# Optimization experiments

Hardware: AMD Instinct MI355X
Metric: run time of the kernel (lower is better)

The kernel has to match this reference:

```python
import jax, jax.numpy as jnp
import numpy as np

N = 30000   # nodes
E = 480000  # directed edges (avg degree 16)
CIN = 64    # c_in
CH = 64     # c_hidden

_PARAM_NAMES = ["Wl1","bl1","Wr1","br1","We1","att1","bo1",
                "Wlm","blm","Wrm","brm","Wem","attm","bom",
                "Wl8","bl8","Wr8","br8","We8","att8","bo8"]
_PARAM_SHAPES = [(CIN,CH),(CH,),(CIN,CH),(CH,),(1,CH),(CH,),(CH,),
                 (6,CH,CH),(6,CH),(6,CH,CH),(6,CH),(6,1,CH),(6,CH),(6,CH),
                 (CH,1),(1,),(CH,1),(1,),(1,1),(1,),(1,)]

def setup_inputs() -> dict:
    key = jax.random.key(0)
    ks = jax.random.split(key, 4 + len(_PARAM_NAMES))
    inp = {
        "features": jax.random.normal(ks[0], (N, CIN), dtype=jnp.float32),
        "edge_src": jax.random.randint(ks[1], (E,), 0, N),
        "edge_dst": jax.random.randint(ks[2], (E,), 0, N),
        "edge_weight": jax.random.uniform(ks[3], (E,), dtype=jnp.float32),
    }
    for i, (name, shape) in enumerate(zip(_PARAM_NAMES, _PARAM_SHAPES)):
        inp[name] = jax.random.normal(ks[4 + i], shape, dtype=jnp.float32) * 0.05
    return inp

def _gatv2_layer(x, src, dst, attr, Wl, bl, Wr, br, We, att, bo):
    # PyG GATv2Conv, heads=1, negative_slope=0.2; (src,dst,attr) already include self-loops.
    n = x.shape[0]
    xl = x @ Wl + bl                                  # [N, C] source-side transform (lin_l)
    xr = x @ Wr + br                                  # [N, C] target-side transform (lin_r)
    e = xl[src] + xr[dst] + attr[:, None] * We[0]     # [Ea, C] per-edge pre-activation
    logit = jax.nn.leaky_relu(e, 0.2) @ att           # [Ea]
    m = jax.ops.segment_max(logit, dst, num_segments=n)
    z = jnp.exp(logit - m[dst])                       # stable softmax over each node's in-edges
    s = jax.ops.segment_sum(z, dst, num_segments=n)
    alpha = z / s[dst]                                # [Ea]
    return jax.ops.segment_sum(alpha[:, None] * xl[src], dst, num_segments=n) + bo

def reference(features, edge_src, edge_dst, edge_weight,
              Wl1, bl1, Wr1, br1, We1, att1, bo1,
              Wlm, blm, Wrm, brm, Wem, attm, bom,
              Wl8, bl8, Wr8, br8, We8, att8, bo8):
    n = features.shape[0]
    # add_self_loops=True with fill_value='mean': self-loop attr = mean of incoming edge attrs
    cnt = jax.ops.segment_sum(jnp.ones_like(edge_weight), edge_dst, num_segments=n)
    loop_attr = jax.ops.segment_sum(edge_weight, edge_dst, num_segments=n) / jnp.maximum(cnt, 1.0)
    loops = jnp.arange(n)
    src = jnp.concatenate([edge_src, loops])
    dst = jnp.concatenate([edge_dst, loops])
    attr = jnp.concatenate([edge_weight, loop_attr])
    x = _gatv2_layer(features, src, dst, attr, Wl1, bl1, Wr1, br1, We1, att1, bo1)
    for i in range(6):  # conv2..conv7, structurally identical hidden layers
        x = _gatv2_layer(x, src, dst, attr, Wlm[i], blm[i], Wrm[i], brm[i], Wem[i], attm[i], bom[i])
    x = _gatv2_layer(x, src, dst, attr, Wl8, bl8, Wr8, br8, We8, att8, bo8)  # [N, 1]
    return jnp.mean(x, axis=-2)  # mean pool over nodes -> [1]
```

## Files before the change

kernel.cpp:

```cpp
#include <hip/hip_runtime.h>
#include <hip/hip_fp16.h>
#include <math.h>

#define CH 64

__device__ __forceinline__ void multi_reduce8(const float lv[8], float L[8], int lane) {
  bool b5 = (lane & 32) != 0;
  float r1[4];
#pragma unroll
  for (int j = 0; j < 4; ++j) {
    float keep = b5 ? lv[j + 4] : lv[j];
    float send = b5 ? lv[j] : lv[j + 4];
    r1[j] = keep + __shfl_xor(send, 32, 64);
  }
  bool b4 = (lane & 16) != 0;
  float r2[2];
#pragma unroll
  for (int j = 0; j < 2; ++j) {
    float keep = b4 ? r1[j + 2] : r1[j];
    float send = b4 ? r1[j] : r1[j + 2];
    r2[j] = keep + __shfl_xor(send, 16, 64);
  }
  bool b3 = (lane & 8) != 0;
  float keep = b3 ? r2[1] : r2[0];
  float send = b3 ? r2[0] : r2[1];
  float v = keep + __shfl_xor(send, 8, 64);
  v += __shfl_xor(v, 4, 64);
  v += __shfl_xor(v, 2, 64);
  v += __shfl_xor(v, 1, 64);
#pragma unroll
  for (int j = 0; j < 8; ++j) L[j] = __shfl(v, j * 8, 64);
}

struct AggState {
  float m, s, acc;
};

__device__ __forceinline__ void agg_batch8(const float xv[8], const int2& ed, int e, int nc,
                                           float Wec, float attc, float xrc, int lane,
                                           AggState& st) {
  float lv[8], L[8];
#pragma unroll
  for (int j = 0; j < 8; ++j) {
    float aj = __int_as_float(__shfl(ed.y, e + j, 64));
    float ee = fmaf(aj, Wec, xv[j] + xrc);
    lv[j] = (ee > 0.f ? ee : 0.2f * ee) * attc;
  }
  multi_reduce8(lv, L, lane);
#pragma unroll
  for (int j = 0; j < 8; ++j)
    if (e + j >= nc) L[j] = -INFINITY;
  float bm = fmaxf(fmaxf(fmaxf(L[0], L[1]), fmaxf(L[2], L[3])),
                   fmaxf(fmaxf(L[4], L[5]), fmaxf(L[6], L[7])));
  float mn = fmaxf(st.m, bm);
  float sc = __expf(st.m - mn);
  float psum = 0.f, pdot = 0.f;
#pragma unroll
  for (int j = 0; j < 8; ++j) {
    float p = __expf(L[j] - mn);
    psum += p;
    pdot = fmaf(p, xv[j], pdot);
  }
  st.s = fmaf(st.s, sc, psum);
  st.acc = fmaf(st.acc, sc, pdot);
  st.m = mn;
}

#define LOAD8(dst, ebase)                                          \
  {                                                                \
    _Pragma("unroll") for (int j = 0; j < 8; ++j) {                \
      int sj = __shfl(ed.x, (ebase) + j, 64);                      \
      dst[j] = __half2float(xlh[(size_t)sj * CH + lane]);          \
    }                                                              \
  }

__device__ __forceinline__ AggState agg_node(const __half* __restrict__ xlh,
                                             const int2* __restrict__ csr, int beg, int dv,
                                             float Wec, float attc, float xrc, int lane) {
  AggState st;
  st.m = -INFINITY;
  st.s = 0.f;
  st.acc = 0.f;
  for (int chunk = 0; chunk < dv; chunk += 64) {
    int nc = min(64, dv - chunk);
    int2 ed = (lane < nc) ? csr[beg + chunk + lane] : make_int2(0, 0);
    float xva[8], xvb[8];
    LOAD8(xva, 0);
    int e = 0;
    for (;;) {
      if (e + 8 < nc) LOAD8(xvb, e + 8);
      agg_batch8(xva, ed, e, nc, Wec, attc, xrc, lane, st);
      e += 8;
      if (e >= nc) break;
      if (e + 8 < nc) LOAD8(xva, e + 8);
      agg_batch8(xvb, ed, e, nc, Wec, attc, xrc, lane, st);
      e += 8;
      if (e >= nc) break;
    }
  }
  return st;
}


#define WSUM_SCALE 33554432.0f
#define WSUM_MASK 0xFFFFFFFFFFULL

__global__ void k_count(const int* __restrict__ dst, const float* __restrict__ w, int E,
                        unsigned long long* __restrict__ agg, int* __restrict__ rank) {
  int i = blockIdx.x * blockDim.x + threadIdx.x;
  if (i < E) {
    int d = dst[i];
    unsigned long long pk = (1ULL << 40) | (unsigned long long)(w[i] * WSUM_SCALE);
    unsigned long long old = atomicAdd(&agg[d], pk);
    rank[i] = (int)(old >> 40);
  }
}

__global__ void k_alloc(const unsigned long long* __restrict__ agg,
                        float* __restrict__ loop_attr, int* __restrict__ deg,
                        int* __restrict__ row_beg, int* __restrict__ total, int n) {
  int i = blockIdx.x * blockDim.x + threadIdx.x;
  int lane = threadIdx.x & 63;
  int d = 0;
  if (i < n) {
    unsigned long long v = agg[i];
    int c = (int)(v >> 40);
    float ws = (float)(v & WSUM_MASK) * (1.0f / WSUM_SCALE);
    loop_attr[i] = ws / fmaxf((float)c, 1.0f);
    d = c + 1;
    deg[i] = d;
  }
  int x = d;
#pragma unroll
  for (int off = 1; off < 64; off <<= 1) {
    int t = __shfl_up(x, off, 64);
    if (lane >= off) x += t;
  }
  int base = 0;
  if (lane == 63) base = atomicAdd(total, x);
  base = __shfl(base, 63, 64);
  if (i < n) row_beg[i] = base + x - d;
}

__global__ void k_scatter(const int* __restrict__ src, const int* __restrict__ dst,
                          const float* __restrict__ w, const int* __restrict__ rank, int E,
                          const int* __restrict__ row_beg, int2* __restrict__ csr) {
  int i = blockIdx.x * blockDim.x + threadIdx.x;
  if (i < E) {
    int d = dst[i];
    csr[row_beg[d] + rank[i]] = make_int2(src[i], __float_as_int(w[i]));
  }
}

__global__ void k_selfloop(int n, const int* __restrict__ row_beg, const int* __restrict__ deg,
                           int2* __restrict__ csr, const float* __restrict__ loop_attr) {
  int v = blockIdx.x * blockDim.x + threadIdx.x;
  if (v < n) {
    csr[row_beg[v] + deg[v] - 1] = make_int2(v, __float_as_int(loop_attr[v]));
  }
}


__global__ void __launch_bounds__(256) k_transform(
    const float* __restrict__ x, const float* __restrict__ Wl, const float* __restrict__ bl,
    const float* __restrict__ Wr, const float* __restrict__ br,
    __half* __restrict__ xlh, float* __restrict__ xr, int n) {
  __shared__ float sW[2][CH * CH];
  for (int i = threadIdx.x; i < (CH * CH) / 4; i += blockDim.x) {
    ((float4*)sW[0])[i] = ((const float4*)Wl)[i];
    ((float4*)sW[1])[i] = ((const float4*)Wr)[i];
  }
  __syncthreads();
  int lane = threadIdx.x & 63;
  int wid = threadIdx.x >> 6;
  float blc = bl[lane], brc = br[lane];
  int wavesPerGrid = (gridDim.x * blockDim.x) >> 6;
  for (int row = blockIdx.x * (blockDim.x >> 6) + wid; row < n; row += wavesPerGrid) {
    float xv = x[(size_t)row * CH + lane];
    float accl = blc, accr = brc;
#pragma unroll
    for (int k = 0; k < CH; ++k) {
      float xk = __shfl(xv, k, 64);
      accl = fmaf(xk, sW[0][k * CH + lane], accl);
      accr = fmaf(xk, sW[1][k * CH + lane], accr);
    }
    xlh[(size_t)row * CH + lane] = __float2half(accl);
    xr[(size_t)row * CH + lane] = accr;
  }
}


__global__ void __launch_bounds__(256) k_aggregate(
    const __half* __restrict__ xlh, const float* __restrict__ xr,
    const int* __restrict__ row_beg, const int* __restrict__ deg,
    const int2* __restrict__ csr,
    const float* __restrict__ We, const float* __restrict__ att, const float* __restrict__ bo,
    float* __restrict__ out, int n) {
  int lane = threadIdx.x & 63;
  int v = (blockIdx.x * blockDim.x + threadIdx.x) >> 6;
  if (v >= n) return;
  float Wec = We[lane], attc = att[lane], boc = bo[lane];
  float xrc = xr[(size_t)v * CH + lane];
  AggState st = agg_node(xlh, csr, row_beg[v], deg[v], Wec, attc, xrc, lane);
  out[(size_t)v * CH + lane] = st.acc / st.s + boc;
}

__global__ void __launch_bounds__(256) k_aggregate_t8(
    const __half* __restrict__ xlh, const float* __restrict__ xr,
    const int* __restrict__ row_beg, const int* __restrict__ deg,
    const int2* __restrict__ csr,
    const float* __restrict__ We, const float* __restrict__ att, const float* __restrict__ bo,
    const float* __restrict__ Wl8, const float* __restrict__ bl8,
    const float* __restrict__ Wr8, const float* __restrict__ br8,
    float* __restrict__ xl8, float* __restrict__ xr8, int n) {
  int lane = threadIdx.x & 63;
  int v = (blockIdx.x * blockDim.x + threadIdx.x) >> 6;
  if (v >= n) return;
  float Wec = We[lane], attc = att[lane], boc = bo[lane];
  float xrc = xr[(size_t)v * CH + lane];
  AggState st = agg_node(xlh, csr, row_beg[v], deg[v], Wec, attc, xrc, lane);
  float orow = st.acc / st.s + boc;
  float a = orow * Wl8[lane];
  float b = orow * Wr8[lane];
#pragma unroll
  for (int off = 32; off > 0; off >>= 1) {
    a += __shfl_xor(a, off, 64);
    b += __shfl_xor(b, off, 64);
  }
  if (lane == 0) {
    xl8[v] = a + bl8[0];
    xr8[v] = b + br8[0];
  }
}

__global__ void __launch_bounds__(256) k_agg8_mean(
    const float* __restrict__ xl8, const float* __restrict__ xr8,
    const int* __restrict__ row_beg, const int* __restrict__ deg,
    const int2* __restrict__ csr,
    const float* __restrict__ We, const float* __restrict__ att, const float* __restrict__ bo,
    float* __restrict__ out, int n) {
  int lane = threadIdx.x & 63;
  int wid = threadIdx.x >> 6;
  float We0 = We[0], att0 = att[0], bo0 = bo[0];
  float inv_n = 1.0f / (float)n;
  float local = 0.f;
  int nwaves = gridDim.x * 4;
  for (int v = blockIdx.x * 4 + wid; v < n; v += nwaves) {
    float xrc = xr8[v];
    int beg = row_beg[v], dv = deg[v];
    float m = -INFINITY, s = 0.f, acc = 0.f;
    for (int chunk = 0; chunk < dv; chunk += 64) {
      int idx = chunk + lane;
      bool valid = idx < dv;
      int2 ed = valid ? csr[beg + idx] : make_int2(0, 0);
      float xlc = valid ? xl8[ed.x] : 0.f;
      float ee = fmaf(__int_as_float(ed.y), We0, xlc + xrc);
      float logit = valid ? (ee > 0.f ? ee : 0.2f * ee) * att0 : -INFINITY;
      float bm = logit;
#pragma unroll
      for (int off = 32; off > 0; off >>= 1) bm = fmaxf(bm, __shfl_xor(bm, off, 64));
      float mn = fmaxf(m, bm);
      float p = __expf(logit - mn);
      float pd = p * xlc;
#pragma unroll
      for (int off = 32; off > 0; off >>= 1) {
        p += __shfl_xor(p, off, 64);
        pd += __shfl_xor(pd, off, 64);
      }
      float sc = __expf(m - mn);
      s = fmaf(s, sc, p);
      acc = fmaf(acc, sc, pd);
      m = mn;
    }
    local += (acc / s + bo0) * inv_n;
  }
  __shared__ float sw[4];
  if (lane == 0) sw[wid] = local;
  __syncthreads();
  if (threadIdx.x == 0) atomicAdd(out, sw[0] + sw[1] + sw[2] + sw[3]);
}


extern "C" void kernel_launch(void* const* d_in, const int* in_sizes, int n_in,
                              void* d_out, int out_size, void* d_ws, size_t ws_size,
                              hipStream_t stream) {
  const float* features = (const float*)d_in[0];
  const int* edge_src = (const int*)d_in[1];
  const int* edge_dst = (const int*)d_in[2];
  const float* edge_w = (const float*)d_in[3];
  const int N = in_sizes[0] / CH;
  const int E = in_sizes[1];

  char* p = (char*)d_ws;
  auto take = [&](size_t bytes) {
    char* r = p;
    p += (bytes + 255) & ~(size_t)255;
    return r;
  };
  float* xA = (float*)take((size_t)N * CH * 4);
  float* xB = (float*)take((size_t)N * CH * 4);
  __half* xlh = (__half*)take((size_t)N * CH * 2);
  float* xr = (float*)take((size_t)N * CH * 4);
  int2* csr = (int2*)take((size_t)(E + N) * 8);
  char* zero_region = take((size_t)N * 8 + 256);
  unsigned long long* agg = (unsigned long long*)zero_region;
  int* total = (int*)(zero_region + (size_t)N * 8);
  int* rank = (int*)take((size_t)E * 4);
  float* loop_attr = (float*)take((size_t)N * 4);
  int* deg = (int*)take((size_t)N * 4);
  int* row_beg = (int*)take((size_t)N * 4);
  float* xl8 = (float*)take((size_t)N * 4);
  float* xr8 = (float*)take((size_t)N * 4);

  hipMemsetAsync(zero_region, 0, (size_t)N * 8 + 256, stream);
  hipMemsetAsync(d_out, 0, sizeof(float), stream);

  const int tb = 256;
  k_count<<<(E + tb - 1) / tb, tb, 0, stream>>>(edge_dst, edge_w, E, agg, rank);
  k_alloc<<<(N + tb - 1) / tb, tb, 0, stream>>>(agg, loop_attr, deg, row_beg, total, N);
  k_scatter<<<(E + tb - 1) / tb, tb, 0, stream>>>(edge_src, edge_dst, edge_w, rank, E,
                                                  row_beg, csr);
  k_selfloop<<<(N + tb - 1) / tb, tb, 0, stream>>>(N, row_beg, deg, csr, loop_attr);

  const float* Wl1 = (const float*)d_in[4];
  const float* bl1 = (const float*)d_in[5];
  const float* Wr1 = (const float*)d_in[6];
  const float* br1 = (const float*)d_in[7];
  const float* We1 = (const float*)d_in[8];
  const float* att1 = (const float*)d_in[9];
  const float* bo1 = (const float*)d_in[10];
  const float* Wlm = (const float*)d_in[11];
  const float* blm = (const float*)d_in[12];
  const float* Wrm = (const float*)d_in[13];
  const float* brm = (const float*)d_in[14];
  const float* Wem = (const float*)d_in[15];
  const float* attm = (const float*)d_in[16];
  const float* bom = (const float*)d_in[17];

  const int agg_grid = ((size_t)N * 64 + tb - 1) / tb;
  const float* x_cur = features;
  float* x_nxt = xA;
  for (int layer = 0; layer < 7; ++layer) {
    const float *Wl, *bl, *Wr, *br, *We, *att, *bo;
    if (layer == 0) {
      Wl = Wl1; bl = bl1; Wr = Wr1; br = br1; We = We1; att = att1; bo = bo1;
    } else {
      int i = layer - 1;
      Wl = Wlm + (size_t)i * CH * CH;
      bl = blm + (size_t)i * CH;
      Wr = Wrm + (size_t)i * CH * CH;
      br = brm + (size_t)i * CH;
      We = Wem + (size_t)i * CH;
      att = attm + (size_t)i * CH;
      bo = bom + (size_t)i * CH;
    }
    k_transform<<<1024, 256, 0, stream>>>(x_cur, Wl, bl, Wr, br, xlh, xr, N);
    if (layer < 6) {
      k_aggregate<<<agg_grid, tb, 0, stream>>>(xlh, xr, row_beg, deg, csr, We, att, bo,
                                               x_nxt, N);
      x_cur = x_nxt;
      x_nxt = (x_nxt == xA) ? xB : xA;
    } else {
      k_aggregate_t8<<<agg_grid, tb, 0, stream>>>(
          xlh, xr, row_beg, deg, csr, We, att, bo, (const float*)d_in[18],
          (const float*)d_in[19], (const float*)d_in[20], (const float*)d_in[21], xl8, xr8, N);
    }
  }
  k_agg8_mean<<<1024, 256, 0, stream>>>(xl8, xr8, row_beg, deg, csr, (const float*)d_in[22],
                                        (const float*)d_in[23], (const float*)d_in[24],
                                        (float*)d_out, N);
}
```

Measured before the change: 631.3 us.

## Remap aggregation wave to 8 edges x 8 channel groups with vectorized gathers

The aggregation kernels now split each 64-lane wave into 8 edge slots by 8 channel groups. Each lane gathers 8 contiguous fp16 features with one 16-byte load, and the CSR entry is read per lane instead of being broadcast by shuffles. The logit reduction becomes a 3-step xor-shuffle within each edge group, and the max and sum across edges use 3 shuffles each. The goal is fewer shuffles and wider memory transactions per edge, at the cost of 8 accumulator registers per lane and a final cross-group reduction of the accumulators.

```diff
diff --git a/kernel.cpp b/kernel.cpp
--- a/kernel.cpp
+++ b/kernel.cpp
@@ -4,102 +4,105 @@
 
 #define CH 64
 
-__device__ __forceinline__ void multi_reduce8(const float lv[8], float L[8], int lane) {
-  bool b5 = (lane & 32) != 0;
-  float r1[4];
+
+struct AggS {
+  float acc[8];
+  float m, s;
+};
+
+__device__ __forceinline__ void gather8(const __half* __restrict__ xlh, int src, int cg,
+                                        float xv[8]) {
+  uint4 raw = *reinterpret_cast<const uint4*>(xlh + ((size_t)src << 6) + (cg << 3));
+  const __half2* h = reinterpret_cast<const __half2*>(&raw);
 #pragma unroll
   for (int j = 0; j < 4; ++j) {
-    float keep = b5 ? lv[j + 4] : lv[j];
-    float send = b5 ? lv[j] : lv[j + 4];
-    r1[j] = keep + __shfl_xor(send, 32, 64);
-  }
-  bool b4 = (lane & 16) != 0;
-  float r2[2];
-#pragma unroll
-  for (int j = 0; j < 2; ++j) {
-    float keep = b4 ? r1[j + 2] : r1[j];
-    float send = b4 ? r1[j] : r1[j + 2];
-    r2[j] = keep + __shfl_xor(send, 16, 64);
-  }
-  bool b3 = (lane & 8) != 0;
-  float keep = b3 ? r2[1] : r2[0];
-  float send = b3 ? r2[0] : r2[1];
-  float v = keep + __shfl_xor(send, 8, 64);
-  v += __shfl_xor(v, 4, 64);
-  v += __shfl_xor(v, 2, 64);
-  v += __shfl_xor(v, 1, 64);
-#pragma unroll
-  for (int j = 0; j < 8; ++j) L[j] = __shfl(v, j * 8, 64);
-}
-
-struct AggState {
-  float m, s, acc;
-};
-
-__device__ __forceinline__ void agg_batch8(const float xv[8], const int2& ed, int e, int nc,
-                                           float Wec, float attc, float xrc, int lane,
-                                           AggState& st) {
-  float lv[8], L[8];
+    float2 f = __half22float2(h[j]);
+    xv[2 * j] = f.x;
+    xv[2 * j + 1] = f.y;
+  }
+}
+
+__device__ __forceinline__ void batch_update(const float xv[8], float a, bool valid,
+                                             const float xrw[8], const float Wec[8],
+                                             const float attc[8], AggS& st) {
+  float partial = 0.f;
 #pragma unroll
   for (int j = 0; j < 8; ++j) {
-    float aj = __int_as_float(__shfl(ed.y, e + j, 64));
-    float ee = fmaf(aj, Wec, xv[j] + xrc);
-    lv[j] = (ee > 0.f ? ee : 0.2f * ee) * attc;
-  }
-  multi_reduce8(lv, L, lane);
-#pragma unroll
-  for (int j = 0; j < 8; ++j)
-    if (e + j >= nc) L[j] = -INFINITY;
-  float bm = fmaxf(fmaxf(fmaxf(L[0], L[1]), fmaxf(L[2], L[3])),
-                   fmaxf(fmaxf(L[4], L[5]), fmaxf(L[6], L[7])));
+    float ee = fmaf(a, Wec[j], xv[j] + xrw[j]);
+    float lr = fmaxf(ee, 0.f) + 0.2f * fminf(ee, 0.f);
+    partial = fmaf(lr, attc[j], partial);
+  }
+  partial += __shfl_xor(partial, 1, 64);
+  partial += __shfl_xor(partial, 2, 64);
+  partial += __shfl_xor(partial, 4, 64);
+  float logit = valid ? partial : -INFINITY;
+  float bm = logit;
+  bm = fmaxf(bm, __shfl_xor(bm, 8, 64));
+  bm = fmaxf(bm, __shfl_xor(bm, 16, 64));
+  bm = fmaxf(bm, __shfl_xor(bm, 32, 64));
   float mn = fmaxf(st.m, bm);
   float sc = __expf(st.m - mn);
-  float psum = 0.f, pdot = 0.f;
+  float p = __expf(logit - mn);
+  float ps = p;
+  ps += __shfl_xor(ps, 8, 64);
+  ps += __shfl_xor(ps, 16, 64);
+  ps += __shfl_xor(ps, 32, 64);
+  st.s = fmaf(st.s, sc, ps);
+#pragma unroll
+  for (int j = 0; j < 8; ++j) st.acc[j] = fmaf(st.acc[j], sc, p * xv[j]);
+  st.m = mn;
+}
+
+__device__ __forceinline__ void agg_node8(const __half* __restrict__ xlh,
+                                          const int2* __restrict__ csr, int beg, int dv,
+                                          const float xrw[8], const float Wec[8],
+                                          const float attc[8], int eg, int cg, AggS& st) {
+  int end = beg + dv;
+  int nb = (dv + 7) >> 3;
+  int idx0 = beg + eg;
+  bool vA = idx0 < end;
+  int2 edA = csr[min(idx0, end - 1)];
+  float xvA[8];
+  gather8(xlh, edA.x, cg, xvA);
+  int2 edB = edA;
+  bool vB = false;
+  if (nb > 1) {
+    int idx1 = beg + 8 + eg;
+    vB = idx1 < end;
+    edB = csr[min(idx1, end - 1)];
+  }
+  for (int t = 0; t < nb; ++t) {
+    float xvB[8];
+    bool haveNext = (t + 1 < nb);
+    if (haveNext) gather8(xlh, edB.x, cg, xvB);
+    int2 edC = edB;
+    bool vC = false;
+    if (t + 2 < nb) {
+      int idx = beg + (t + 2) * 8 + eg;
+      vC = idx < end;
+      edC = csr[min(idx, end - 1)];
+    }
+    batch_update(xvA, __int_as_float(edA.y), vA, xrw, Wec, attc, st);
+    edA = edB; vA = vB;
+    edB = edC; vB = vC;
+    if (haveNext) {
+#pragma unroll
+      for (int j = 0; j < 8; ++j) xvA[j] = xvB[j];
+    }
+  }
 #pragma unroll
   for (int j = 0; j < 8; ++j) {
-    float p = __expf(L[j] - mn);
-    psum += p;
-    pdot = fmaf(p, xv[j], pdot);
-  }
-  st.s = fmaf(st.s, sc, psum);
-  st.acc = fmaf(st.acc, sc, pdot);
-  st.m = mn;
-}
-
-#define LOAD8(dst, ebase)                                          \
-  {                                                                \
-    _Pragma("unroll") for (int j = 0; j < 8; ++j) {                \
-      int sj = __shfl(ed.x, (ebase) + j, 64);                      \
-      dst[j] = __half2float(xlh[(size_t)sj * CH + lane]);          \
-    }                                                              \
-  }
-
-__device__ __forceinline__ AggState agg_node(const __half* __restrict__ xlh,
-                                             const int2* __restrict__ csr, int beg, int dv,
-                                             float Wec, float attc, float xrc, int lane) {
-  AggState st;
-  st.m = -INFINITY;
-  st.s = 0.f;
-  st.acc = 0.f;
-  for (int chunk = 0; chunk < dv; chunk += 64) {
-    int nc = min(64, dv - chunk);
-    int2 ed = (lane < nc) ? csr[beg + chunk + lane] : make_int2(0, 0);
-    float xva[8], xvb[8];
-    LOAD8(xva, 0);
-    int e = 0;
-    for (;;) {
-      if (e + 8 < nc) LOAD8(xvb, e + 8);
-      agg_batch8(xva, ed, e, nc, Wec, attc, xrc, lane, st);
-      e += 8;
-      if (e >= nc) break;
-      if (e + 8 < nc) LOAD8(xva, e + 8);
-      agg_batch8(xvb, ed, e, nc, Wec, attc, xrc, lane, st);
-      e += 8;
-      if (e >= nc) break;
-    }
-  }
-  return st;
-}
+    st.acc[j] += __shfl_xor(st.acc[j], 8, 64);
+    st.acc[j] += __shfl_xor(st.acc[j], 16, 64);
+    st.acc[j] += __shfl_xor(st.acc[j], 32, 64);
+  }
+}
+
+#define LOAD8F(dst, srcp)                                \
+  {                                                      \
+    *(float4*)&dst[0] = *(const float4*)&(srcp)[0];      \
+    *(float4*)&dst[4] = *(const float4*)&(srcp)[4];      \
+  }
 
 
 #define WSUM_SCALE 33554432.0f
@@ -199,10 +202,27 @@
   int lane = threadIdx.x & 63;
   int v = (blockIdx.x * blockDim.x + threadIdx.x) >> 6;
   if (v >= n) return;
-  float Wec = We[lane], attc = att[lane], boc = bo[lane];
-  float xrc = xr[(size_t)v * CH + lane];
-  AggState st = agg_node(xlh, csr, row_beg[v], deg[v], Wec, attc, xrc, lane);
-  out[(size_t)v * CH + lane] = st.acc / st.s + boc;
+  int eg = lane >> 3, cg = lane & 7;
+  int c0 = cg << 3;
+  float Wec[8], attc[8], xrw[8];
+  LOAD8F(Wec, We + c0);
+  LOAD8F(attc, att + c0);
+  LOAD8F(xrw, xr + (size_t)v * CH + c0);
+  AggS st;
+  st.m = -INFINITY;
+  st.s = 0.f;
+#pragma unroll
+  for (int j = 0; j < 8; ++j) st.acc[j] = 0.f;
+  agg_node8(xlh, csr, row_beg[v], deg[v], xrw, Wec, attc, eg, cg, st);
+  if (eg == 0) {
+    float boc[8];
+    LOAD8F(boc, bo + c0);
+    float o[8];
+#pragma unroll
+    for (int j = 0; j < 8; ++j) o[j] = st.acc[j] / st.s + boc[j];
+    *(float4*)&out[(size_t)v * CH + c0] = *(float4*)&o[0];
+    *(float4*)&out[(size_t)v * CH + c0 + 4] = *(float4*)&o[4];
+  }
 }
 
 __global__ void __launch_bounds__(256) k_aggregate_t8(
@@ -216,20 +236,38 @@
   int lane = threadIdx.x & 63;
   int v = (blockIdx.x * blockDim.x + threadIdx.x) >> 6;
   if (v >= n) return;
-  float Wec = We[lane], attc = att[lane], boc = bo[lane];
-  float xrc = xr[(size_t)v * CH + lane];
-  AggState st = agg_node(xlh, csr, row_beg[v], deg[v], Wec, attc, xrc, lane);
-  float orow = st.acc / st.s + boc;
-  float a = orow * Wl8[lane];
-  float b = orow * Wr8[lane];
-#pragma unroll
-  for (int off = 32; off > 0; off >>= 1) {
-    a += __shfl_xor(a, off, 64);
-    b += __shfl_xor(b, off, 64);
-  }
+  int eg = lane >> 3, cg = lane & 7;
+  int c0 = cg << 3;
+  float Wec[8], attc[8], xrw[8];
+  LOAD8F(Wec, We + c0);
+  LOAD8F(attc, att + c0);
+  LOAD8F(xrw, xr + (size_t)v * CH + c0);
+  AggS st;
+  st.m = -INFINITY;
+  st.s = 0.f;
+#pragma unroll
+  for (int j = 0; j < 8; ++j) st.acc[j] = 0.f;
+  agg_node8(xlh, csr, row_beg[v], deg[v], xrw, Wec, attc, eg, cg, st);
+  float boc[8], wl8c[8], wr8c[8];
+  LOAD8F(boc, bo + c0);
+  LOAD8F(wl8c, Wl8 + c0);
+  LOAD8F(wr8c, Wr8 + c0);
+  float pa = 0.f, pb = 0.f;
+#pragma unroll
+  for (int j = 0; j < 8; ++j) {
+    float o = st.acc[j] / st.s + boc[j];
+    pa = fmaf(o, wl8c[j], pa);
+    pb = fmaf(o, wr8c[j], pb);
+  }
+  pa += __shfl_xor(pa, 1, 64);
+  pa += __shfl_xor(pa, 2, 64);
+  pa += __shfl_xor(pa, 4, 64);
+  pb += __shfl_xor(pb, 1, 64);
+  pb += __shfl_xor(pb, 2, 64);
+  pb += __shfl_xor(pb, 4, 64);
   if (lane == 0) {
-    xl8[v] = a + bl8[0];
-    xr8[v] = b + br8[0];
+    xl8[v] = pa + bl8[0];
+    xr8[v] = pb + br8[0];
   }
 }
 
```

After: 581.8 us. -7.8%, faster.
